# Performance work log

Hardware: AMD Instinct MI355X
Metric: run time of the kernel (lower is better)

## Reference

```python
import jax, jax.numpy as jnp
import numpy as np

N, E, D, H, G = 50000, 640000, 128, 128, 64
EPS = 1e-5


def gcn_conv(x, row, col, W, b, n):
    # PyG GCNConv: linear transform, symmetric deg^-1/2 normalization (self-loops
    # already appended to row/col), scatter-add aggregation, then bias.
    h = x @ W  # [N, H]
    ones = jnp.ones(row.shape[0], dtype=h.dtype)
    deg = jax.ops.segment_sum(ones, col, num_segments=n)
    dinv = jnp.where(deg > 0, jax.lax.rsqrt(deg), 0.0)
    norm = dinv[row] * dinv[col]                       # [E+N]
    msg = h[row] * norm[:, None]                       # gather + scale
    out = jax.ops.segment_sum(msg, col, num_segments=n)  # scatter-add
    return out + b


def graph_layernorm(x, w, b):
    # PyG LayerNorm(mode='graph') with batch=None: normalize over the whole tensor.
    mu = x.mean()
    xc = x - mu
    std = jnp.sqrt((xc * xc).mean())
    return xc / (std + EPS) * w + b


def setup_inputs() -> dict:
    key = jax.random.key(0)
    ks = jax.random.split(key, 12)
    x = jax.random.normal(ks[0], (N, D), dtype=jnp.float32)
    edge_index = jax.random.randint(ks[1], (2, E), 0, N, dtype=jnp.int64)
    batch = jnp.sort(jax.random.randint(ks[2], (N,), 0, G, dtype=jnp.int64))
    s1 = 1.0 / np.sqrt(D)
    s2 = 1.0 / np.sqrt(H)
    return {
        "x": x,
        "edge_index": edge_index,
        "batch": batch,
        "W1": jax.random.normal(ks[3], (D, H), dtype=jnp.float32) * s1,
        "b1": jnp.zeros((H,), dtype=jnp.float32),
        "ln1_w": jnp.ones((H,), dtype=jnp.float32),
        "ln1_b": jnp.zeros((H,), dtype=jnp.float32),
        "W2": jax.random.normal(ks[4], (H, H), dtype=jnp.float32) * s2,
        "b2": jnp.zeros((H,), dtype=jnp.float32),
        "ln2_w": jnp.ones((H,), dtype=jnp.float32),
        "ln2_b": jnp.zeros((H,), dtype=jnp.float32),
        "fc_w": jax.random.normal(ks[5], (H, 1), dtype=jnp.float32) * s2,
        "fc_b": jnp.zeros((1,), dtype=jnp.float32),
    }


def reference(x, edge_index, batch, W1, b1, ln1_w, ln1_b, W2, b2, ln2_w, ln2_b, fc_w, fc_b):
    n = x.shape[0]
    loops = jnp.arange(n, dtype=edge_index.dtype)
    row = jnp.concatenate([edge_index[0], loops])  # add self-loops
    col = jnp.concatenate([edge_index[1], loops])

    h = gcn_conv(x, row, col, W1, b1, n)
    h = jax.nn.relu(graph_layernorm(h, ln1_w, ln1_b))
    h = gcn_conv(h, row, col, W2, b2, n)
    h = jax.nn.relu(graph_layernorm(h, ln2_w, ln2_b))

    # global_mean_pool over batch segment ids
    sums = jax.ops.segment_sum(h, batch, num_segments=G)          # [G, H]
    cnt = jax.ops.segment_sum(jnp.ones((n,), h.dtype), batch, num_segments=G)
    pooled = sums / jnp.maximum(cnt, 1.0)[:, None]

    logits = pooled @ fc_w + fc_b                                  # [G, 1]
    return jax.nn.sigmoid(logits).squeeze(-1)                      # [G]
```

## Files before the change

kernel.cpp:

```cpp
#include <hip/hip_runtime.h>
#include <math.h>

#define H 128
#define PC 16

typedef _Float16 half8v __attribute__((ext_vector_type(8)));
typedef float floatx4 __attribute__((ext_vector_type(4)));

__device__ __forceinline__ int lower_bound_i(const int* a, int n, int key) {
  int lo = 0, hi = n;
  while (lo < hi) { int mid = (lo + hi) >> 1; if (a[mid] < key) lo = mid + 1; else hi = mid; }
  return lo;
}

__global__ void k_init(const float* __restrict__ W1, const float* __restrict__ W2,
                       _Float16* __restrict__ PW1, _Float16* __restrict__ PW2,
                       int* cntE, float* slots, int* esrc,
                       float* glog, int* gdone, int* total,
                       int cap, int n, int g) {
  int b = blockIdx.x;
  int tid = threadIdx.x;
  if (b < 128) {
    int t = b * 256 + tid;
    const float* W = (t < 16384) ? W1 : W2;
    _Float16* PW = (t < 16384) ? PW1 : PW2;
    int u = t & 16383;
    int j = u & 7;
    int nn = (u >> 3) & 15;
    int quad = (u >> 7) & 3;
    int ks = (u >> 9) & 3;
    int ct = (u >> 11) & 7;
    PW[u] = (_Float16)W[(ks * 32 + quad * 8 + j) * H + ct * 16 + nn];
  } else {
    int i = (b - 128) * 256 + tid;
    int stride = 128 * 256;
    for (int j = i; j < n; j += stride) cntE[j] = 0;
    for (int j = i; j < 256; j += stride) slots[j] = 0.f;
    for (int j = i; j < cap; j += stride) esrc[j] = n;
    for (int j = i; j < g; j += stride) { glog[j] = 0.f; gdone[j] = 0; }
    if (i == 0) *total = 0;
  }
}

__device__ __forceinline__ void gemm_tile_raw(const float* __restrict__ Xf,
                                              const _Float16* __restrict__ PW,
                                              _Float16* __restrict__ O,
                                              int wave, int laneid, int n) {
  int m = laneid & 15;
  int quad = laneid >> 4;
  int r0 = wave * 16;
  int row = r0 + m;
  if (row >= n) row = n - 1;
  floatx4 acc[8] = {};
  const half8v* PB8 = (const half8v*)PW;
#pragma unroll
  for (int ks = 0; ks < 4; ks++) {
    int kb = ks * 32 + quad * 8;
    const float* xr = Xf + (size_t)row * H + kb;
    float4 u0 = *(const float4*)xr;
    float4 u1 = *(const float4*)(xr + 4);
    half8v a;
    a[0] = (_Float16)u0.x; a[1] = (_Float16)u0.y; a[2] = (_Float16)u0.z; a[3] = (_Float16)u0.w;
    a[4] = (_Float16)u1.x; a[5] = (_Float16)u1.y; a[6] = (_Float16)u1.z; a[7] = (_Float16)u1.w;
#pragma unroll
    for (int ct = 0; ct < 8; ct++) {
      half8v b = PB8[((ct * 4 + ks) * 4 + quad) * 16 + m];
      acc[ct] = __builtin_amdgcn_mfma_f32_16x16x32_f16(a, b, acc[ct], 0, 0, 0);
    }
  }
#pragma unroll
  for (int ct = 0; ct < 8; ct++) {
#pragma unroll
    for (int reg = 0; reg < 4; reg++) {
      int ro = r0 + quad * 4 + reg;
      if (ro < n) O[(size_t)ro * H + ct * 16 + m] = (_Float16)acc[ct][reg];
    }
  }
}

__global__ __launch_bounds__(256) void k_cg1(const float* __restrict__ Xf,
                                             const _Float16* __restrict__ PW,
                                             _Float16* __restrict__ O,
                                             const int* __restrict__ col,
                                             int* __restrict__ cntE, int* __restrict__ perm,
                                             int E, int n, int GB) {
  int b = blockIdx.x;
  if (b < GB) {
    if (b == 0 && threadIdx.x < 16) {
      half8v z = {};
      *(half8v*)&O[(size_t)n * H + threadIdx.x * 8] = z;
    }
    int wave = b * 4 + (threadIdx.x >> 6);
    int tiles = (n + 15) >> 4;
    if (wave >= tiles) return;
    gemm_tile_raw(Xf, PW, O, wave, threadIdx.x & 63, n);
  } else {
    int e = (b - GB) * 256 + threadIdx.x;
    if (e < E) perm[e] = atomicAdd(&cntE[col[e]], 1);
  }
}

__global__ void k_alloc(const int* __restrict__ cntE, int* __restrict__ offs,
                        float* __restrict__ dinv, int* __restrict__ total, int n) {
  int i = blockIdx.x * 256 + threadIdx.x;
  if (i < n) {
    int c = cntE[i];
    offs[i] = atomicAdd(total, (c + 15) & ~15);
    dinv[i] = rsqrtf((float)(c + 1));
  } else if (i == n) {
    dinv[n] = 0.f;
  }
}

__global__ void k_scat(const int* __restrict__ row, const int* __restrict__ col,
                       const int* __restrict__ offs, const int* __restrict__ perm,
                       int* __restrict__ esrc, int E) {
  int e = blockIdx.x * 256 + threadIdx.x;
  if (e < E) esrc[offs[col[e]] + perm[e]] = row[e];
}

template<int WEIGHTED>
__global__ __launch_bounds__(256) void k_agg(const _Float16* __restrict__ Gs,
                                             _Float16* __restrict__ Out,
                                             const int* __restrict__ esrc, const int* __restrict__ offs,
                                             const int* __restrict__ cntE, const float* __restrict__ dinv,
                                             const float* __restrict__ bias, float* __restrict__ slot,
                                             int n) {
  int sub = threadIdx.x >> 4;
  int lane = threadIdx.x & 15;
  int i = blockIdx.x * 16 + sub;
  float sv = 0.f, sq = 0.f;
  if (i < n) {
    float di = dinv[i];
    half8v gself = *(const half8v*)&Gs[(size_t)i * H + 8 * lane];
    float acc[8];
#pragma unroll
    for (int e = 0; e < 8; e++) acc[e] = WEIGHTED ? di * (float)gself[e] : (float)gself[e];
    int beg = offs[i];
    int c16 = (cntE[i] + 15) & ~15;
    int sid = (c16 > 0) ? esrc[beg + lane] : 0;
    float dvp = WEIGHTED ? dinv[sid] : 0.f;
    for (int base = 0; base < c16; base += 16) {
      int cur = sid;
      float dvc = dvp;
      if (base + 16 < c16) {
        sid = esrc[beg + base + 16 + lane];
        if (WEIGHTED) dvp = dinv[sid];
      }
      int sg[16]; half8v hg[16]; float dg[16];
#pragma unroll
      for (int u = 0; u < 16; u++) sg[u] = __shfl(cur, u, 16);
      if (WEIGHTED) {
#pragma unroll
        for (int u = 0; u < 16; u++) dg[u] = __shfl(dvc, u, 16);
      }
#pragma unroll
      for (int u = 0; u < 16; u++) hg[u] = *(const half8v*)&Gs[(size_t)sg[u] * H + 8 * lane];
#pragma unroll
      for (int e = 0; e < 8; e++) {
        float t0 = 0.f, t1 = 0.f;
        if (WEIGHTED) {
#pragma unroll
          for (int u = 0; u < 8; u++) { t0 += dg[u] * (float)hg[u][e]; t1 += dg[8 + u] * (float)hg[8 + u][e]; }
        } else {
#pragma unroll
          for (int u = 0; u < 8; u++) { t0 += (float)hg[u][e]; t1 += (float)hg[8 + u][e]; }
        }
        acc[e] += t0 + t1;
      }
    }
    const float* bb = bias + 8 * lane;
    half8v vo;
#pragma unroll
    for (int e = 0; e < 8; e++) {
      float v = di * acc[e] + bb[e];
      vo[e] = (_Float16)v;
      sv += v;
      sq += v * v;
    }
    *(half8v*)&Out[(size_t)i * H + 8 * lane] = vo;
  }
#pragma unroll
  for (int o = 32; o > 0; o >>= 1) {
    sv += __shfl_xor(sv, o, 64);
    sq += __shfl_xor(sq, o, 64);
  }
  __shared__ float rsm[4], rqm[4];
  int wave = threadIdx.x >> 6;
  if ((threadIdx.x & 63) == 0) { rsm[wave] = sv; rqm[wave] = sq; }
  __syncthreads();
  if (threadIdx.x == 0) {
    float ts = rsm[0] + rsm[1] + rsm[2] + rsm[3];
    float tq = rqm[0] + rqm[1] + rqm[2] + rqm[3];
    int sl = blockIdx.x & 63;
    atomicAdd(&slot[sl], ts);
    atomicAdd(&slot[64 + sl], tq);
  }
}

__global__ __launch_bounds__(256) void k_gemm2(const _Float16* __restrict__ Xh,
                                               const _Float16* __restrict__ PW,
                                               const float* __restrict__ lnw,
                                               const float* __restrict__ lnb,
                                               const float* __restrict__ slot, float invM,
                                               const float* __restrict__ dinv,
                                               _Float16* __restrict__ O, int n) {
  if (blockIdx.x == 0 && threadIdx.x < 16) {
    half8v z = {};
    *(half8v*)&O[(size_t)n * H + threadIdx.x * 8] = z;
  }
  int wave = blockIdx.x * 4 + (threadIdx.x >> 6);
  int tiles = (n + 15) >> 4;
  if (wave >= tiles) return;
  int lane = threadIdx.x & 63;
  int m = lane & 15;
  int quad = lane >> 4;
  int r0 = wave * 16;
  int row = r0 + m;
  if (row >= n) row = n - 1;

  float s = slot[lane], q = slot[64 + lane];
#pragma unroll
  for (int o = 32; o > 0; o >>= 1) { s += __shfl_xor(s, o, 64); q += __shfl_xor(q, o, 64); }
  float mu = s * invM;
  float var = fmaxf(q * invM - mu * mu, 0.f);
  float rs = 1.f / (sqrtf(var) + 1e-5f);

  floatx4 acc[8] = {};
  const half8v* PB8 = (const half8v*)PW;
#pragma unroll
  for (int ks = 0; ks < 4; ks++) {
    int kb = ks * 32 + quad * 8;
    half8v hv = *(const half8v*)(Xh + (size_t)row * H + kb);
    float4 w0 = *(const float4*)(lnw + kb);
    float4 w1 = *(const float4*)(lnw + kb + 4);
    float4 c0 = *(const float4*)(lnb + kb);
    float4 c1 = *(const float4*)(lnb + kb + 4);
    half8v a;
    a[0] = (_Float16)fmaxf(((float)hv[0] - mu) * rs * w0.x + c0.x, 0.f);
    a[1] = (_Float16)fmaxf(((float)hv[1] - mu) * rs * w0.y + c0.y, 0.f);
    a[2] = (_Float16)fmaxf(((float)hv[2] - mu) * rs * w0.z + c0.z, 0.f);
    a[3] = (_Float16)fmaxf(((float)hv[3] - mu) * rs * w0.w + c0.w, 0.f);
    a[4] = (_Float16)fmaxf(((float)hv[4] - mu) * rs * w1.x + c1.x, 0.f);
    a[5] = (_Float16)fmaxf(((float)hv[5] - mu) * rs * w1.y + c1.y, 0.f);
    a[6] = (_Float16)fmaxf(((float)hv[6] - mu) * rs * w1.z + c1.z, 0.f);
    a[7] = (_Float16)fmaxf(((float)hv[7] - mu) * rs * w1.w + c1.w, 0.f);
#pragma unroll
    for (int ct = 0; ct < 8; ct++) {
      half8v b = PB8[((ct * 4 + ks) * 4 + quad) * 16 + m];
      acc[ct] = __builtin_amdgcn_mfma_f32_16x16x32_f16(a, b, acc[ct], 0, 0, 0);
    }
  }
  float dv[4];
#pragma unroll
  for (int reg = 0; reg < 4; reg++) {
    int ro = r0 + quad * 4 + reg;
    dv[reg] = (ro < n) ? dinv[ro] : 0.f;
  }
#pragma unroll
  for (int ct = 0; ct < 8; ct++) {
#pragma unroll
    for (int reg = 0; reg < 4; reg++) {
      int ro = r0 + quad * 4 + reg;
      if (ro < n) O[(size_t)ro * H + ct * 16 + m] = (_Float16)(acc[ct][reg] * dv[reg]);
    }
  }
}

__global__ __launch_bounds__(128) void k_poolfc(const _Float16* __restrict__ Hs,
                                                const int* __restrict__ batch,
                                                const float* __restrict__ lnw, const float* __restrict__ lnb,
                                                const float* __restrict__ slot, float invM,
                                                const float* __restrict__ fcw, const float* __restrict__ fcb,
                                                float* __restrict__ glog, int* __restrict__ gdone,
                                                float* __restrict__ out, int n) {
  int g = blockIdx.x / PC, q = blockIdx.x % PC;
  int t = threadIdx.x;
  int l = t & 63;
  float s = slot[l], qq = slot[64 + l];
#pragma unroll
  for (int o = 32; o > 0; o >>= 1) { s += __shfl_xor(s, o, 64); qq += __shfl_xor(qq, o, 64); }
  float mu = s * invM;
  float var = fmaxf(qq * invM - mu * mu, 0.f);
  float rs = 1.f / (sqrtf(var) + 1e-5f);

  int start = lower_bound_i(batch, n, g);
  int end = lower_bound_i(batch, n, g + 1);
  int tot = end - start;
  int per = (tot + PC - 1) / PC;
  int s0 = start + q * per;
  int e0 = s0 + per; if (e0 > end) e0 = end;
  float w = lnw[t], bb = lnb[t];
  float acc = 0.f;
  for (int i = s0; i < e0; i++) {
    float v = (float)Hs[(size_t)i * H + t];
    v = (v - mu) * rs * w + bb;
    acc += fmaxf(v, 0.f);
  }
  float cnt = fmaxf((float)tot, 1.f);
  float v = acc * fcw[t] / cnt;
  int wave = t >> 6;
#pragma unroll
  for (int o = 32; o > 0; o >>= 1) v += __shfl_xor(v, o, 64);
  __shared__ float r2[2];
  if (l == 0) r2[wave] = v;
  __syncthreads();
  if (t == 0) {
    float part = r2[0] + r2[1];
    atomicAdd(&glog[g], part);
    __threadfence();
    int old = atomicAdd(&gdone[g], 1);
    if (old == PC - 1) {
      float totv = atomicAdd(&glog[g], 0.0f);
      out[g] = 1.f / (1.f + expf(-(totv + fcb[0])));
    }
  }
}

extern "C" void kernel_launch(void* const* d_in, const int* in_sizes, int n_in,
                              void* d_out, int out_size, void* d_ws, size_t ws_size,
                              hipStream_t stream) {
  const float* x    = (const float*)d_in[0];
  const int*   ei   = (const int*)d_in[1];
  const int*   batch= (const int*)d_in[2];
  const float* W1   = (const float*)d_in[3];
  const float* b1   = (const float*)d_in[4];
  const float* ln1w = (const float*)d_in[5];
  const float* ln1b = (const float*)d_in[6];
  const float* W2   = (const float*)d_in[7];
  const float* b2   = (const float*)d_in[8];
  const float* ln2w = (const float*)d_in[9];
  const float* ln2b = (const float*)d_in[10];
  const float* fcw  = (const float*)d_in[11];
  const float* fcb  = (const float*)d_in[12];
  float* out = (float*)d_out;

  int N = in_sizes[2];
  int E = in_sizes[1] / 2;
  int G = out_size;
  int CAP = E + 15 * N;

  char* p = (char*)d_ws;
  int*   cntE   = (int*)p;   p += (size_t)N * 4;
  int*   offs   = (int*)p;   p += (size_t)N * 4;
  float* dinv   = (float*)p; p += (size_t)(N + 1) * 4;
  int*   perm   = (int*)p;   p += (size_t)E * 4;
  int*   esrc   = (int*)p;   p += (size_t)CAP * 4;
  _Float16* bufA = (_Float16*)p; p += (size_t)(N + 1) * H * 2;
  _Float16* bufB = (_Float16*)p; p += (size_t)(N + 1) * H * 2;
  _Float16* PW1  = (_Float16*)p; p += 16384 * 2;
  _Float16* PW2  = (_Float16*)p; p += 16384 * 2;
  float* slots  = (float*)p; p += 256 * 4;
  float* glog   = (float*)p; p += (size_t)G * 4;
  int*   gdone  = (int*)p;   p += (size_t)G * 4;
  int*   total  = (int*)p;   p += 4;

  const int* row = ei;
  const int* col = ei + E;

  int EB = (E + 255) / 256;
  int tiles = (N + 15) / 16;
  int GB = (tiles + 3) / 4;
  float invM = 1.f / ((float)N * (float)H);

  k_init<<<256, 256, 0, stream>>>(W1, W2, PW1, PW2, cntE, slots, esrc, glog, gdone, total, CAP, N, G);
  k_cg1<<<GB + EB, 256, 0, stream>>>(x, PW1, bufA, col, cntE, perm, E, N, GB);
  k_alloc<<<(N + 1 + 255) / 256, 256, 0, stream>>>(cntE, offs, dinv, total, N);
  k_scat<<<EB, 256, 0, stream>>>(row, col, offs, perm, esrc, E);
  k_agg<1><<<(N + 15) / 16, 256, 0, stream>>>(bufA, bufB, esrc, offs, cntE, dinv, b1, slots, N);
  k_gemm2<<<GB, 256, 0, stream>>>(bufB, PW2, ln1w, ln1b, slots, invM, dinv, bufA, N);
  k_agg<0><<<(N + 15) / 16, 256, 0, stream>>>(bufA, bufB, esrc, offs, cntE, dinv, b2, slots + 128, N);
  k_poolfc<<<G * PC, 128, 0, stream>>>(bufB, batch, ln2w, ln2b, slots + 128, invM, fcw, fcb,
                                       glog, gdone, out, N);
}
```

Before: 280.7 us.

## Prescale layer-1 GEMM output by dinv and fuse scatter with GEMM

Reorders the pipeline so edge counting and offset allocation run before the first GEMM. The GEMM epilogue can then multiply each row by its deg^-1/2 factor, and the first aggregation drops its per-edge dinv gathers and multiplies by using the unweighted path. The edge scatter now shares a launch with the first GEMM. k_alloc is rewritten to do a block-level prefix scan with one atomic per block instead of one atomic per node. The trade-off is that the counting atomics no longer overlap with the GEMM.

```diff
diff --git a/kernel.cpp b/kernel.cpp
--- a/kernel.cpp
+++ b/kernel.cpp
@@ -42,8 +42,48 @@
   }
 }
 
-__device__ __forceinline__ void gemm_tile_raw(const float* __restrict__ Xf,
+__global__ void k_count(const int* __restrict__ col, int* __restrict__ cntE,
+                        int* __restrict__ perm, int E) {
+  int e = blockIdx.x * blockDim.x + threadIdx.x;
+  if (e < E) perm[e] = atomicAdd(&cntE[col[e]], 1);
+}
+
+__global__ __launch_bounds__(256) void k_alloc(const int* __restrict__ cnt,
+                                               int* __restrict__ offs,
+                                               float* __restrict__ dinv,
+                                               int* __restrict__ total, int n) {
+  __shared__ int ws[4];
+  __shared__ int base_sh;
+  int tid = threadIdx.x;
+  int i = blockIdx.x * 256 + tid;
+  int c = (i < n) ? cnt[i] : 0;
+  int v = (i < n) ? ((c + 15) & ~15) : 0;
+  int lane = tid & 63;
+  int wid = tid >> 6;
+  int incl = v;
+#pragma unroll
+  for (int o = 1; o < 64; o <<= 1) {
+    int t = __shfl_up(incl, o, 64);
+    if (lane >= o) incl += t;
+  }
+  if (lane == 63) ws[wid] = incl;
+  __syncthreads();
+  if (tid == 0) {
+    int s = 0;
+#pragma unroll
+    for (int w = 0; w < 4; w++) { int t = ws[w]; ws[w] = s; s += t; }
+    base_sh = atomicAdd(total, s);
+  }
+  __syncthreads();
+  if (i < n) {
+    offs[i] = base_sh + ws[wid] + (incl - v);
+    dinv[i] = rsqrtf((float)(c + 1));
+  }
+}
+
+__device__ __forceinline__ void gemm_tile_f32(const float* __restrict__ Xf,
                                               const _Float16* __restrict__ PW,
+                                              const float* __restrict__ dinv,
                                               _Float16* __restrict__ O,
                                               int wave, int laneid, int n) {
   int m = laneid & 15;
@@ -68,22 +108,29 @@
       acc[ct] = __builtin_amdgcn_mfma_f32_16x16x32_f16(a, b, acc[ct], 0, 0, 0);
     }
   }
+  float dv[4];
+#pragma unroll
+  for (int reg = 0; reg < 4; reg++) {
+    int ro = r0 + quad * 4 + reg;
+    dv[reg] = (ro < n) ? dinv[ro] : 0.f;
+  }
 #pragma unroll
   for (int ct = 0; ct < 8; ct++) {
 #pragma unroll
     for (int reg = 0; reg < 4; reg++) {
       int ro = r0 + quad * 4 + reg;
-      if (ro < n) O[(size_t)ro * H + ct * 16 + m] = (_Float16)acc[ct][reg];
-    }
-  }
-}
-
-__global__ __launch_bounds__(256) void k_cg1(const float* __restrict__ Xf,
+      if (ro < n) O[(size_t)ro * H + ct * 16 + m] = (_Float16)(acc[ct][reg] * dv[reg]);
+    }
+  }
+}
+
+__global__ __launch_bounds__(256) void k_sg1(const int* __restrict__ row, const int* __restrict__ col,
+                                             const int* __restrict__ offs, const int* __restrict__ perm,
+                                             int* __restrict__ esrc, int E,
+                                             const float* __restrict__ Xf,
                                              const _Float16* __restrict__ PW,
-                                             _Float16* __restrict__ O,
-                                             const int* __restrict__ col,
-                                             int* __restrict__ cntE, int* __restrict__ perm,
-                                             int E, int n, int GB) {
+                                             const float* __restrict__ dinv,
+                                             _Float16* __restrict__ O, int n, int GB) {
   int b = blockIdx.x;
   if (b < GB) {
     if (b == 0 && threadIdx.x < 16) {
@@ -93,33 +140,16 @@
     int wave = b * 4 + (threadIdx.x >> 6);
     int tiles = (n + 15) >> 4;
     if (wave >= tiles) return;
-    gemm_tile_raw(Xf, PW, O, wave, threadIdx.x & 63, n);
+    gemm_tile_f32(Xf, PW, dinv, O, wave, threadIdx.x & 63, n);
   } else {
     int e = (b - GB) * 256 + threadIdx.x;
-    if (e < E) perm[e] = atomicAdd(&cntE[col[e]], 1);
-  }
-}
-
-__global__ void k_alloc(const int* __restrict__ cntE, int* __restrict__ offs,
-                        float* __restrict__ dinv, int* __restrict__ total, int n) {
-  int i = blockIdx.x * 256 + threadIdx.x;
-  if (i < n) {
-    int c = cntE[i];
-    offs[i] = atomicAdd(total, (c + 15) & ~15);
-    dinv[i] = rsqrtf((float)(c + 1));
-  } else if (i == n) {
-    dinv[n] = 0.f;
-  }
-}
-
-__global__ void k_scat(const int* __restrict__ row, const int* __restrict__ col,
-                       const int* __restrict__ offs, const int* __restrict__ perm,
-                       int* __restrict__ esrc, int E) {
-  int e = blockIdx.x * 256 + threadIdx.x;
-  if (e < E) esrc[offs[col[e]] + perm[e]] = row[e];
-}
-
-template<int WEIGHTED>
+    if (e < E) {
+      int c = col[e];
+      esrc[offs[c] + perm[e]] = row[e];
+    }
+  }
+}
+
 __global__ __launch_bounds__(256) void k_agg(const _Float16* __restrict__ Gs,
                                              _Float16* __restrict__ Out,
                                              const int* __restrict__ esrc, const int* __restrict__ offs,
@@ -135,37 +165,23 @@
     half8v gself = *(const half8v*)&Gs[(size_t)i * H + 8 * lane];
     float acc[8];
 #pragma unroll
-    for (int e = 0; e < 8; e++) acc[e] = WEIGHTED ? di * (float)gself[e] : (float)gself[e];
+    for (int e = 0; e < 8; e++) acc[e] = (float)gself[e];
     int beg = offs[i];
     int c16 = (cntE[i] + 15) & ~15;
     int sid = (c16 > 0) ? esrc[beg + lane] : 0;
-    float dvp = WEIGHTED ? dinv[sid] : 0.f;
     for (int base = 0; base < c16; base += 16) {
       int cur = sid;
-      float dvc = dvp;
-      if (base + 16 < c16) {
-        sid = esrc[beg + base + 16 + lane];
-        if (WEIGHTED) dvp = dinv[sid];
-      }
-      int sg[16]; half8v hg[16]; float dg[16];
+      if (base + 16 < c16) sid = esrc[beg + base + 16 + lane];
+      int sg[16]; half8v hg[16];
 #pragma unroll
       for (int u = 0; u < 16; u++) sg[u] = __shfl(cur, u, 16);
-      if (WEIGHTED) {
-#pragma unroll
-        for (int u = 0; u < 16; u++) dg[u] = __shfl(dvc, u, 16);
-      }
 #pragma unroll
       for (int u = 0; u < 16; u++) hg[u] = *(const half8v*)&Gs[(size_t)sg[u] * H + 8 * lane];
 #pragma unroll
       for (int e = 0; e < 8; e++) {
         float t0 = 0.f, t1 = 0.f;
-        if (WEIGHTED) {
-#pragma unroll
-          for (int u = 0; u < 8; u++) { t0 += dg[u] * (float)hg[u][e]; t1 += dg[8 + u] * (float)hg[8 + u][e]; }
-        } else {
-#pragma unroll
-          for (int u = 0; u < 8; u++) { t0 += (float)hg[u][e]; t1 += (float)hg[8 + u][e]; }
-        }
+#pragma unroll
+        for (int u = 0; u < 8; u++) { t0 += (float)hg[u][e]; t1 += (float)hg[8 + u][e]; }
         acc[e] += t0 + t1;
       }
     }
@@ -343,7 +359,7 @@
   char* p = (char*)d_ws;
   int*   cntE   = (int*)p;   p += (size_t)N * 4;
   int*   offs   = (int*)p;   p += (size_t)N * 4;
-  float* dinv   = (float*)p; p += (size_t)(N + 1) * 4;
+  float* dinv   = (float*)p; p += (size_t)N * 4;
   int*   perm   = (int*)p;   p += (size_t)E * 4;
   int*   esrc   = (int*)p;   p += (size_t)CAP * 4;
   _Float16* bufA = (_Float16*)p; p += (size_t)(N + 1) * H * 2;
@@ -359,17 +375,18 @@
   const int* col = ei + E;
 
   int EB = (E + 255) / 256;
+  int NB = (N + 255) / 256;
   int tiles = (N + 15) / 16;
   int GB = (tiles + 3) / 4;
   float invM = 1.f / ((float)N * (float)H);
 
   k_init<<<256, 256, 0, stream>>>(W1, W2, PW1, PW2, cntE, slots, esrc, glog, gdone, total, CAP, N, G);
-  k_cg1<<<GB + EB, 256, 0, stream>>>(x, PW1, bufA, col, cntE, perm, E, N, GB);
-  k_alloc<<<(N + 1 + 255) / 256, 256, 0, stream>>>(cntE, offs, dinv, total, N);
-  k_scat<<<EB, 256, 0, stream>>>(row, col, offs, perm, esrc, E);
-  k_agg<1><<<(N + 15) / 16, 256, 0, stream>>>(bufA, bufB, esrc, offs, cntE, dinv, b1, slots, N);
+  k_count<<<EB, 256, 0, stream>>>(col, cntE, perm, E);
+  k_alloc<<<NB, 256, 0, stream>>>(cntE, offs, dinv, total, N);
+  k_sg1<<<GB + EB, 256, 0, stream>>>(row, col, offs, perm, esrc, E, x, PW1, dinv, bufA, N, GB);
+  k_agg<<<(N + 15) / 16, 256, 0, stream>>>(bufA, bufB, esrc, offs, cntE, dinv, b1, slots, N);
   k_gemm2<<<GB, 256, 0, stream>>>(bufB, PW2, ln1w, ln1b, slots, invM, dinv, bufA, N);
-  k_agg<0><<<(N + 15) / 16, 256, 0, stream>>>(bufA, bufB, esrc, offs, cntE, dinv, b2, slots + 128, N);
+  k_agg<<<(N + 15) / 16, 256, 0, stream>>>(bufA, bufB, esrc, offs, cntE, dinv, b2, slots + 128, N);
   k_poolfc<<<G * PC, 128, 0, stream>>>(bufB, batch, ln2w, ln2b, slots + 128, invM, fcw, fcb,
                                        glog, gdone, out, N);
 }
```

Result: faster. 267.3 us (-4.8%).
